# Kernel optimization log

Measured on AMD Instinct MI355X. Metric: run time of the kernel, lower is better.

Reference implementation:

```python
import jax, jax.numpy as jnp
import numpy as np

N_NODES = 100000
N_EDGES = 3200000
IN_CH = 32
EDGE_DIM = 8
HEADS = 8
HIDDEN = 64


def _lin(key, fan_in, fan_out, bias=True):
    k1, k2 = jax.random.split(key)
    s = 1.0 / np.sqrt(fan_in)
    w = jax.random.uniform(k1, (fan_in, fan_out), jnp.float32, -s, s)
    if bias:
        b = jax.random.uniform(k2, (fan_out,), jnp.float32, -s, s)
        return w, b
    return w


def setup_inputs() -> dict:
    key = jax.random.key(0)
    ks = jax.random.split(key, 40)
    inp = {}
    inp['x'] = jax.random.normal(ks[0], (N_NODES, IN_CH), jnp.float32)
    inp['edge_index'] = jax.random.randint(ks[1], (2, N_EDGES), 0, N_NODES, jnp.int32)
    inp['edge_attr'] = jax.random.normal(ks[2], (N_EDGES, EDGE_DIM), jnp.float32)
    # layer dims: (in, heads, out_per_head)
    dims = [(IN_CH, HEADS, 6), (HEADS * 6, HEADS, 3), (HEADS * 3, 1, HIDDEN)]
    ki = 3
    for li, (cin, H, C) in enumerate(dims, start=1):
        HC = H * C
        inp[f'wq{li}'], inp[f'bq{li}'] = _lin(ks[ki], cin, HC); ki += 1
        inp[f'wk{li}'], inp[f'bk{li}'] = _lin(ks[ki], cin, HC); ki += 1
        inp[f'wv{li}'], inp[f'bv{li}'] = _lin(ks[ki], cin, HC); ki += 1
        inp[f'we{li}'] = _lin(ks[ki], EDGE_DIM, HC, bias=False); ki += 1
        inp[f'wskip{li}'], inp[f'bskip{li}'] = _lin(ks[ki], cin, HC); ki += 1
        inp[f'wbeta{li}'] = _lin(ks[ki], 3 * HC, 1, bias=False); ki += 1
    inp['wc'], inp['bc'] = _lin(ks[ki], HIDDEN, 1)
    return inp


def _transformer_conv(x, src, dst, edge_attr, wq, bq, wk, bk, wv, bv, we, wskip, bskip, wbeta, H, C):
    """PyG TransformerConv (concat=True, beta=True, root_weight=True), eval mode."""
    N = x.shape[0]
    e = (edge_attr @ we).reshape(-1, H, C)                  # [E,H,C]
    q = (x @ wq + bq).reshape(N, H, C)[dst]                 # [E,H,C]
    k = (x @ wk + bk).reshape(N, H, C)[src] + e
    v = (x @ wv + bv).reshape(N, H, C)[src] + e
    logits = (q * k).sum(-1) * (1.0 / np.sqrt(C))           # [E,H]
    # segment softmax over incoming edges of each dst node
    m = jax.ops.segment_max(logits, dst, num_segments=N)
    ex = jnp.exp(logits - m[dst])
    den = jax.ops.segment_sum(ex, dst, num_segments=N)
    alpha = ex / (den[dst] + 1e-16)                         # [E,H]
    out = jax.ops.segment_sum(alpha[:, :, None] * v, dst, num_segments=N)
    out = out.reshape(N, H * C)
    x_r = x @ wskip + bskip
    g = jax.nn.sigmoid(jnp.concatenate([out, x_r, out - x_r], axis=-1) @ wbeta)  # [N,1]
    return g * x_r + (1.0 - g) * out


def reference(x, edge_index, edge_attr,
              wq1, bq1, wk1, bk1, wv1, bv1, we1, wskip1, bskip1, wbeta1,
              wq2, bq2, wk2, bk2, wv2, bv2, we2, wskip2, bskip2, wbeta2,
              wq3, bq3, wk3, bk3, wv3, bv3, we3, wskip3, bskip3, wbeta3,
              wc, bc):
    src, dst = edge_index[0], edge_index[1]
    h = _transformer_conv(x, src, dst, edge_attr, wq1, bq1, wk1, bk1, wv1, bv1, we1, wskip1, bskip1, wbeta1, HEADS, 6)
    h = jax.nn.relu(h)
    h = _transformer_conv(h, src, dst, edge_attr, wq2, bq2, wk2, bk2, wv2, bv2, we2, wskip2, bskip2, wbeta2, HEADS, 3)
    h = jax.nn.relu(h)
    h = _transformer_conv(h, src, dst, edge_attr, wq3, bq3, wk3, bk3, wv3, bv3, we3, wskip3, bskip3, wbeta3, 1, HIDDEN)
    h = jax.nn.relu(h)
    logits = (h @ wc + bc).squeeze(-1)                      # [N]
    return logits
```

## Files before the change

### kernel.cpp

```cpp
#include <hip/hip_runtime.h>
#include <hip/hip_fp16.h>
#include <math.h>

#define RCHUNK 8192
#define NBUCK 512
#define CAP 12288

__device__ __forceinline__ float2 H2F(unsigned u) {
    __half2 h = *reinterpret_cast<__half2*>(&u);
    return __half22float2(h);
}
__device__ __forceinline__ unsigned F2H(float a, float b) {
    __half2 h = __floats2half2_rn(a, b);
    return *reinterpret_cast<unsigned*>(&h);
}

__device__ __forceinline__ void loadA(const __half* p, float* a) {
    uint4 u = *(const uint4*)p;
    float2 t;
    t = H2F(u.x); a[0] = t.x; a[1] = t.y;
    t = H2F(u.y); a[2] = t.x; a[3] = t.y;
    t = H2F(u.z); a[4] = t.x; a[5] = t.y;
    t = H2F(u.w); a[6] = t.x; a[7] = t.y;
}

template<int C>
__device__ __forceinline__ void loadKV(const __half* p, float* k, float* v) {
    if constexpr (C == 6) {
        uint4 p0 = *(const uint4*)p;
        uint4 p1 = *(const uint4*)(p + 8);
        float2 t;
        t = H2F(p0.x); k[0] = t.x; k[1] = t.y;
        t = H2F(p0.y); k[2] = t.x; k[3] = t.y;
        t = H2F(p0.z); k[4] = t.x; k[5] = t.y;
        t = H2F(p0.w); v[0] = t.x; v[1] = t.y;
        t = H2F(p1.x); v[2] = t.x; v[3] = t.y;
        t = H2F(p1.y); v[4] = t.x; v[5] = t.y;
    } else {
        uint4 p0 = *(const uint4*)p;
        float2 t;
        t = H2F(p0.x); k[0] = t.x; k[1] = t.y;
        t = H2F(p0.y); k[2] = t.x; v[0] = t.y;
        t = H2F(p0.z); v[1] = t.x; v[2] = t.y;
    }
}

__global__ void histA_kernel(const int* __restrict__ ei, int* __restrict__ hist,
                             int E, int nblk) {
    __shared__ int h[NBUCK];
    h[threadIdx.x] = 0;
    h[threadIdx.x + 256] = 0;
    __syncthreads();
    int base = blockIdx.x * RCHUNK;
#pragma unroll
    for (int r = 0; r < RCHUNK / 256; ++r) {
        int i = base + r * 256 + threadIdx.x;
        if (i < E) atomicAdd(&h[ei[E + i] >> 8], 1);
    }
    __syncthreads();
    hist[threadIdx.x * nblk + blockIdx.x] = h[threadIdx.x];
    hist[(threadIdx.x + 256) * nblk + blockIdx.x] = h[threadIdx.x + 256];
}

__global__ void scanB_kernel(int* __restrict__ hist, int* __restrict__ btot, int nblk) {
    __shared__ int sm[1024];
    int b = blockIdx.x;
    int tid = threadIdx.x;
    int v = (tid < nblk) ? hist[b * nblk + tid] : 0;
    sm[tid] = v;
    __syncthreads();
    for (int off = 1; off < 1024; off <<= 1) {
        int t = (tid >= off) ? sm[tid - off] : 0;
        __syncthreads();
        sm[tid] += t;
        __syncthreads();
    }
    if (tid < nblk) hist[b * nblk + tid] = sm[tid] - v;
    if (tid == 1023) btot[b] = sm[1023];
}

__global__ void scanC_kernel(const int* __restrict__ btot, int* __restrict__ bbase) {
    __shared__ int sm[NBUCK];
    int tid = threadIdx.x;
    int v = btot[tid];
    sm[tid] = v;
    __syncthreads();
    for (int off = 1; off < NBUCK; off <<= 1) {
        int t = (tid >= off) ? sm[tid - off] : 0;
        __syncthreads();
        sm[tid] += t;
        __syncthreads();
    }
    bbase[tid] = sm[tid] - v;
}

__global__ void reorderB_kernel(const int* __restrict__ ei, const int* __restrict__ hist,
                                const int* __restrict__ bbase, unsigned* __restrict__ sorted,
                                int E, int nblk) {
    __shared__ int off[NBUCK];
    off[threadIdx.x] = bbase[threadIdx.x] + hist[threadIdx.x * nblk + blockIdx.x];
    off[threadIdx.x + 256] = bbase[threadIdx.x + 256] + hist[(threadIdx.x + 256) * nblk + blockIdx.x];
    __syncthreads();
    int base = blockIdx.x * RCHUNK;
#pragma unroll
    for (int r = 0; r < RCHUNK / 256; ++r) {
        int i = base + r * 256 + threadIdx.x;
        if (i < E) {
            int dst = ei[E + i];
            int k = atomicAdd(&off[dst >> 8], 1);
            sorted[k] = ((unsigned)(dst & 255) << 24) | (unsigned)i;
        }
    }
}

__global__ __launch_bounds__(256) void bucketsort_kernel(
        const unsigned* __restrict__ sorted,
        const int* __restrict__ bbase, const int* __restrict__ btot,
        int* __restrict__ rowptr,
        const int* __restrict__ ei, const float* __restrict__ ea,
        int* __restrict__ srcp, __half* __restrict__ eap, int N, int E) {
    __shared__ int h[256];
    __shared__ int tmp[CAP];
    int b = blockIdx.x;
    int lo = b << 8;
    int s = bbase[b], cnt = btot[b];
    int tid = threadIdx.x;

    h[tid] = 0;
    __syncthreads();
    for (int i = tid; i < cnt; i += 256) atomicAdd(&h[sorted[s + i] >> 24], 1);
    __syncthreads();
    int v = h[tid];
    for (int off = 1; off < 256; off <<= 1) {
        int t = (tid >= off) ? h[tid - off] : 0;
        __syncthreads();
        h[tid] += t;
        __syncthreads();
    }
    int excl = h[tid] - v;
    int dst = lo + tid;
    if (dst < N) rowptr[dst] = s + excl;
    if (b == 0 && tid == 0) rowptr[N] = E;
    __syncthreads();
    h[tid] = excl;
    __syncthreads();
    for (int i = tid; i < cnt; i += 256) {
        unsigned p2 = sorted[s + i];
        int dl = p2 >> 24;
        int eid = p2 & 0xFFFFFF;
        int r = atomicAdd(&h[dl], 1);
        if (r < CAP) {
            tmp[r] = eid;
        } else {
            int slot = s + r;
            srcp[slot] = ei[eid];
            float4 a0 = *(const float4*)(ea + (size_t)eid * 8);
            float4 a1 = *(const float4*)(ea + (size_t)eid * 8 + 4);
            uint4 u;
            u.x = F2H(a0.x, a0.y); u.y = F2H(a0.z, a0.w);
            u.z = F2H(a1.x, a1.y); u.w = F2H(a1.z, a1.w);
            *(uint4*)(eap + (size_t)slot * 8) = u;
        }
    }
    __syncthreads();
    int m = cnt < CAP ? cnt : CAP;
    for (int j = tid; j < m; j += 256) {
        int eid = tmp[j];
        int slot = s + j;
        srcp[slot] = ei[eid];
        float4 a0 = *(const float4*)(ea + (size_t)eid * 8);
        float4 a1 = *(const float4*)(ea + (size_t)eid * 8 + 4);
        uint4 u;
        u.x = F2H(a0.x, a0.y); u.y = F2H(a0.z, a0.w);
        u.z = F2H(a1.x, a1.y); u.w = F2H(a1.z, a1.w);
        *(uint4*)(eap + (size_t)slot * 8) = u;
    }
}

template<int CIN, int C, int PK>
__global__ void proj8_kernel(const float* __restrict__ X,
                             const float* __restrict__ wq, const float* __restrict__ bq,
                             const float* __restrict__ wk, const float* __restrict__ bk,
                             const float* __restrict__ wv, const float* __restrict__ bv,
                             const float* __restrict__ wsk, const float* __restrict__ bsk,
                             float* __restrict__ Q, __half* __restrict__ KV,
                             float* __restrict__ S, int N)
{
    const int HC = 8 * C;
    int idx = blockIdx.x * blockDim.x + threadIdx.x;
    if (idx >= N * HC) return;
    int n = idx / HC;
    int c = idx - n * HC;
    int h = c / C;
    int cc = c - h * C;
    float q = bq[c], k = bk[c], v = bv[c], s = bsk[c];
    const float* xr = X + (size_t)n * CIN;
#pragma unroll
    for (int i = 0; i < CIN; ++i) {
        float xi = xr[i];
        q = fmaf(xi, wq[i * HC + c], q);
        k = fmaf(xi, wk[i * HC + c], k);
        v = fmaf(xi, wv[i * HC + c], v);
        s = fmaf(xi, wsk[i * HC + c], s);
    }
    Q[(size_t)n * HC + c] = q;
    __half* kp = KV + (size_t)n * (8 * PK) + h * PK;
    kp[cc] = __float2half_rn(k);
    kp[C + cc] = __float2half_rn(v);
    S[(size_t)n * HC + c] = s;
}

__global__ void proj64_kernel(const float* __restrict__ X,
                              const float* __restrict__ wq, const float* __restrict__ bq,
                              const float* __restrict__ wk, const float* __restrict__ bk,
                              const float* __restrict__ wv, const float* __restrict__ bv,
                              const float* __restrict__ wsk, const float* __restrict__ bsk,
                              float* __restrict__ Q, __half* __restrict__ K16,
                              __half* __restrict__ V16, float* __restrict__ S, int N)
{
    int idx = blockIdx.x * blockDim.x + threadIdx.x;
    if (idx >= N * 64) return;
    int n = idx >> 6;
    int c = idx & 63;
    float q = bq[c], k = bk[c], v = bv[c], s = bsk[c];
    const float* xr = X + (size_t)n * 24;
#pragma unroll
    for (int i = 0; i < 24; ++i) {
        float xi = xr[i];
        q = fmaf(xi, wq[i * 64 + c], q);
        k = fmaf(xi, wk[i * 64 + c], k);
        v = fmaf(xi, wv[i * 64 + c], v);
        s = fmaf(xi, wsk[i * 64 + c], s);
    }
    Q[idx] = q;
    K16[idx] = __float2half_rn(k);
    V16[idx] = __float2half_rn(v);
    S[idx] = s;
}

template<int C, int PK, int UNR>
__global__ void gather8f_kernel(const int* __restrict__ rowptr,
                                const int* __restrict__ srcp,
                                const __half* __restrict__ eap,
                                const float* __restrict__ we,
                                const float* __restrict__ Q,
                                const __half* __restrict__ KV,
                                const float* __restrict__ S,
                                const float* __restrict__ wb,
                                float* __restrict__ OUT,
                                int N, float scale)
{
    const int HC = 8 * C;
    int tid = blockIdx.x * blockDim.x + threadIdx.x;
    int n = tid >> 3;
    int h = tid & 7;
    if (n >= N) return;

    float q[C];
    const float* Qp = Q + (size_t)n * HC + h * C;
#pragma unroll
    for (int c = 0; c < C; ++c) q[c] = Qp[c];

    float qe[8];
#pragma unroll
    for (int d = 0; d < 8; ++d) {
        float t = 0.f;
#pragma unroll
        for (int c = 0; c < C; ++c) t = fmaf(we[d * HC + h * C + c], q[c], t);
        qe[d] = t;
    }

    float num[C];
#pragma unroll
    for (int c = 0; c < C; ++c) num[c] = 0.f;
    float sacc[8];
#pragma unroll
    for (int d = 0; d < 8; ++d) sacc[d] = 0.f;
    float den = 0.f;

    int rs = rowptr[n], re = rowptr[n + 1];
    int j = rs;
    for (; j + UNR - 1 < re; j += UNR) {
        int se[UNR];
        float a[UNR][8], kk[UNR][C], vv[UNR][C];
#pragma unroll
        for (int u = 0; u < UNR; ++u) se[u] = srcp[j + u];
#pragma unroll
        for (int u = 0; u < UNR; ++u) loadA(eap + (size_t)(j + u) * 8, a[u]);
#pragma unroll
        for (int u = 0; u < UNR; ++u)
            loadKV<C>(KV + (size_t)se[u] * (8 * PK) + h * PK, kk[u], vv[u]);
        float ex[UNR];
#pragma unroll
        for (int u = 0; u < UNR; ++u) {
            float d0 = 0.f;
#pragma unroll
            for (int c = 0; c < C; ++c) d0 = fmaf(q[c], kk[u][c], d0);
            float qa = 0.f;
#pragma unroll
            for (int d = 0; d < 8; ++d) qa = fmaf(qe[d], a[u][d], qa);
            ex[u] = __expf((d0 + qa) * scale);
        }
#pragma unroll
        for (int u = 0; u < UNR; ++u) {
            den += ex[u];
#pragma unroll
            for (int c = 0; c < C; ++c) num[c] = fmaf(ex[u], vv[u][c], num[c]);
#pragma unroll
            for (int d = 0; d < 8; ++d) sacc[d] = fmaf(ex[u], a[u][d], sacc[d]);
        }
    }
    for (; j < re; ++j) {
        int s0 = srcp[j];
        float a0[8];
        loadA(eap + (size_t)j * 8, a0);
        float k0[C], v0[C];
        loadKV<C>(KV + (size_t)s0 * (8 * PK) + h * PK, k0, v0);
        float d0 = 0.f;
#pragma unroll
        for (int c = 0; c < C; ++c) d0 = fmaf(q[c], k0[c], d0);
        float qa0 = 0.f;
#pragma unroll
        for (int d = 0; d < 8; ++d) qa0 = fmaf(qe[d], a0[d], qa0);
        float ex0 = __expf((d0 + qa0) * scale);
        den += ex0;
#pragma unroll
        for (int c = 0; c < C; ++c) num[c] = fmaf(ex0, v0[c], num[c]);
#pragma unroll
        for (int d = 0; d < 8; ++d) sacc[d] = fmaf(ex0, a0[d], sacc[d]);
    }

    float inv = 1.f / (den + 1e-16f);
    float outc[C], sc[C];
    float gd = 0.f;
#pragma unroll
    for (int c = 0; c < C; ++c) {
        float e_ = 0.f;
#pragma unroll
        for (int d = 0; d < 8; ++d) e_ = fmaf(we[d * HC + h * C + c], sacc[d], e_);
        float o = (num[c] + e_) * inv;
        float s_ = S[(size_t)n * HC + h * C + c];
        outc[c] = o;
        sc[c] = s_;
        gd += o * wb[h * C + c] + s_ * wb[HC + h * C + c] + (o - s_) * wb[2 * HC + h * C + c];
    }
    gd += __shfl_xor(gd, 1, 8);
    gd += __shfl_xor(gd, 2, 8);
    gd += __shfl_xor(gd, 4, 8);
    float g = 1.f / (1.f + __expf(-gd));
#pragma unroll
    for (int c = 0; c < C; ++c) {
        float hh = fmaxf(g * sc[c] + (1.f - g) * outc[c], 0.f);
        OUT[(size_t)n * HC + h * C + c] = hh;
    }
}

__global__ __launch_bounds__(256) void gather64f_kernel(
        const int* __restrict__ rowptr,
        const int* __restrict__ srcp,
        const __half* __restrict__ eap,
        const float* __restrict__ we,
        const float* __restrict__ Q,
        const __half* __restrict__ K16,
        const __half* __restrict__ V16,
        const float* __restrict__ S,
        const float* __restrict__ wb,
        const float* __restrict__ wc,
        const float* __restrict__ bc,
        float* __restrict__ OUT,
        int N, float scale)
{
    int grp = (blockIdx.x * blockDim.x + threadIdx.x) >> 3;
    int l8 = threadIdx.x & 7;
    if (grp >= N) return;
    int c0 = l8 << 3;

    float q[8];
    *(float4*)q       = *(const float4*)(Q + (size_t)grp * 64 + c0);
    *(float4*)(q + 4) = *(const float4*)(Q + (size_t)grp * 64 + c0 + 4);
    float qe[8];
#pragma unroll
    for (int d = 0; d < 8; ++d) {
        float4 w0 = *(const float4*)(we + d * 64 + c0);
        float4 w1 = *(const float4*)(we + d * 64 + c0 + 4);
        float t = w0.x * q[0];
        t = fmaf(w0.y, q[1], t); t = fmaf(w0.z, q[2], t); t = fmaf(w0.w, q[3], t);
        t = fmaf(w1.x, q[4], t); t = fmaf(w1.y, q[5], t); t = fmaf(w1.z, q[6], t);
        t = fmaf(w1.w, q[7], t);
        qe[d] = t;
    }

    float num[8];
#pragma unroll
    for (int c = 0; c < 8; ++c) num[c] = 0.f;
    float sacc[8];
#pragma unroll
    for (int d = 0; d < 8; ++d) sacc[d] = 0.f;
    float den = 0.f;

    int rs = rowptr[grp], re = rowptr[grp + 1];
    int j = rs;
    for (; j + 3 < re; j += 4) {
        int se[4];
        float a[4][8];
        uint4 ku[4], vu[4];
#pragma unroll
        for (int u = 0; u < 4; ++u) se[u] = srcp[j + u];
#pragma unroll
        for (int u = 0; u < 4; ++u) loadA(eap + (size_t)(j + u) * 8, a[u]);
#pragma unroll
        for (int u = 0; u < 4; ++u) {
            ku[u] = *(const uint4*)(K16 + (size_t)se[u] * 64 + c0);
            vu[u] = *(const uint4*)(V16 + (size_t)se[u] * 64 + c0);
        }
        float t[4];
#pragma unroll
        for (int u = 0; u < 4; ++u) {
            float2 k01 = H2F(ku[u].x), k23 = H2F(ku[u].y);
            float2 k45 = H2F(ku[u].z), k67 = H2F(ku[u].w);
            float tt = q[0] * k01.x;
            tt = fmaf(q[1], k01.y, tt); tt = fmaf(q[2], k23.x, tt);
            tt = fmaf(q[3], k23.y, tt); tt = fmaf(q[4], k45.x, tt);
            tt = fmaf(q[5], k45.y, tt); tt = fmaf(q[6], k67.x, tt);
            tt = fmaf(q[7], k67.y, tt);
#pragma unroll
            for (int d = 0; d < 8; ++d) tt = fmaf(qe[d], a[u][d], tt);
            t[u] = tt;
        }
#pragma unroll
        for (int off = 4; off > 0; off >>= 1) {
            t[0] += __shfl_xor(t[0], off, 8);
            t[1] += __shfl_xor(t[1], off, 8);
            t[2] += __shfl_xor(t[2], off, 8);
            t[3] += __shfl_xor(t[3], off, 8);
        }
#pragma unroll
        for (int u = 0; u < 4; ++u) {
            float ex = __expf(t[u] * scale);
            den += ex;
            float2 v01 = H2F(vu[u].x), v23 = H2F(vu[u].y);
            float2 v45 = H2F(vu[u].z), v67 = H2F(vu[u].w);
            num[0] = fmaf(ex, v01.x, num[0]);
            num[1] = fmaf(ex, v01.y, num[1]);
            num[2] = fmaf(ex, v23.x, num[2]);
            num[3] = fmaf(ex, v23.y, num[3]);
            num[4] = fmaf(ex, v45.x, num[4]);
            num[5] = fmaf(ex, v45.y, num[5]);
            num[6] = fmaf(ex, v67.x, num[6]);
            num[7] = fmaf(ex, v67.y, num[7]);
#pragma unroll
            for (int d = 0; d < 8; ++d) sacc[d] = fmaf(ex, a[u][d], sacc[d]);
        }
    }
    for (; j < re; ++j) {
        int s0 = srcp[j];
        float a0[8];
        loadA(eap + (size_t)j * 8, a0);
        uint4 ku0 = *(const uint4*)(K16 + (size_t)s0 * 64 + c0);
        uint4 vu0 = *(const uint4*)(V16 + (size_t)s0 * 64 + c0);
        float2 k01 = H2F(ku0.x), k23 = H2F(ku0.y);
        float2 k45 = H2F(ku0.z), k67 = H2F(ku0.w);
        float t0 = q[0] * k01.x;
        t0 = fmaf(q[1], k01.y, t0); t0 = fmaf(q[2], k23.x, t0);
        t0 = fmaf(q[3], k23.y, t0); t0 = fmaf(q[4], k45.x, t0);
        t0 = fmaf(q[5], k45.y, t0); t0 = fmaf(q[6], k67.x, t0);
        t0 = fmaf(q[7], k67.y, t0);
#pragma unroll
        for (int d = 0; d < 8; ++d) t0 = fmaf(qe[d], a0[d], t0);
#pragma unroll
        for (int off = 4; off > 0; off >>= 1) t0 += __shfl_xor(t0, off, 8);
        float ex0 = __expf(t0 * scale);
        den += ex0;
        float2 v01 = H2F(vu0.x), v23 = H2F(vu0.y);
        float2 v45 = H2F(vu0.z), v67 = H2F(vu0.w);
        num[0] = fmaf(ex0, v01.x, num[0]);
        num[1] = fmaf(ex0, v01.y, num[1]);
        num[2] = fmaf(ex0, v23.x, num[2]);
        num[3] = fmaf(ex0, v23.y, num[3]);
        num[4] = fmaf(ex0, v45.x, num[4]);
        num[5] = fmaf(ex0, v45.y, num[5]);
        num[6] = fmaf(ex0, v67.x, num[6]);
        num[7] = fmaf(ex0, v67.y, num[7]);
#pragma unroll
        for (int d = 0; d < 8; ++d) sacc[d] = fmaf(ex0, a0[d], sacc[d]);
    }

#pragma unroll
    for (int d = 0; d < 8; ++d) {
        float4 w0 = *(const float4*)(we + d * 64 + c0);
        float4 w1 = *(const float4*)(we + d * 64 + c0 + 4);
        num[0] = fmaf(w0.x, sacc[d], num[0]);
        num[1] = fmaf(w0.y, sacc[d], num[1]);
        num[2] = fmaf(w0.z, sacc[d], num[2]);
        num[3] = fmaf(w0.w, sacc[d], num[3]);
        num[4] = fmaf(w1.x, sacc[d], num[4]);
        num[5] = fmaf(w1.y, sacc[d], num[5]);
        num[6] = fmaf(w1.z, sacc[d], num[6]);
        num[7] = fmaf(w1.w, sacc[d], num[7]);
    }
    float inv = 1.f / (den + 1e-16f);
    float o[8], sv[8];
    *(float4*)sv       = *(const float4*)(S + (size_t)grp * 64 + c0);
    *(float4*)(sv + 4) = *(const float4*)(S + (size_t)grp * 64 + c0 + 4);
    float gd = 0.f;
#pragma unroll
    for (int c = 0; c < 8; ++c) {
        o[c] = num[c] * inv;
        gd += o[c] * wb[c0 + c] + sv[c] * wb[64 + c0 + c] + (o[c] - sv[c]) * wb[128 + c0 + c];
    }
#pragma unroll
    for (int off = 4; off > 0; off >>= 1) gd += __shfl_xor(gd, off, 8);
    float g = 1.f / (1.f + __expf(-gd));
    float t = 0.f;
#pragma unroll
    for (int c = 0; c < 8; ++c) {
        float hh = fmaxf(g * sv[c] + (1.f - g) * o[c], 0.f);
        t = fmaf(hh, wc[c0 + c], t);
    }
#pragma unroll
    for (int off = 4; off > 0; off >>= 1) t += __shfl_xor(t, off, 8);
    if (l8 == 0) OUT[grp] = t + bc[0];
}

extern "C" void kernel_launch(void* const* d_in, const int* in_sizes, int n_in,
                              void* d_out, int out_size, void* d_ws, size_t ws_size,
                              hipStream_t stream) {
    const float* x  = (const float*)d_in[0];
    const int*   ei = (const int*)d_in[1];
    const float* ea = (const float*)d_in[2];
    const int N = in_sizes[0] / 32;
    const int E = in_sizes[1] / 2;

    int p = 3;
    const float *wq1=(const float*)d_in[p+0], *bq1=(const float*)d_in[p+1],
                *wk1=(const float*)d_in[p+2], *bk1=(const float*)d_in[p+3],
                *wv1=(const float*)d_in[p+4], *bv1=(const float*)d_in[p+5],
                *we1=(const float*)d_in[p+6],
                *wsk1=(const float*)d_in[p+7], *bsk1=(const float*)d_in[p+8],
                *wb1=(const float*)d_in[p+9];
    p += 10;
    const float *wq2=(const float*)d_in[p+0], *bq2=(const float*)d_in[p+1],
                *wk2=(const float*)d_in[p+2], *bk2=(const float*)d_in[p+3],
                *wv2=(const float*)d_in[p+4], *bv2=(const float*)d_in[p+5],
                *we2=(const float*)d_in[p+6],
                *wsk2=(const float*)d_in[p+7], *bsk2=(const float*)d_in[p+8],
                *wb2=(const float*)d_in[p+9];
    p += 10;
    const float *wq3=(const float*)d_in[p+0], *bq3=(const float*)d_in[p+1],
                *wk3=(const float*)d_in[p+2], *bk3=(const float*)d_in[p+3],
                *wv3=(const float*)d_in[p+4], *bv3=(const float*)d_in[p+5],
                *we3=(const float*)d_in[p+6],
                *wsk3=(const float*)d_in[p+7], *bsk3=(const float*)d_in[p+8],
                *wb3=(const float*)d_in[p+9];
    p += 10;
    const float *wc = (const float*)d_in[p+0], *bc = (const float*)d_in[p+1];

    float* out = (float*)d_out;

    float* ws = (float*)d_ws;
    float* Hb = ws;
    float* Qb = Hb + (size_t)N * 48;
    float* Sb = Qb + (size_t)N * 64;
    __half* KV16  = (__half*)(Sb + (size_t)N * 64);
    __half* K3    = KV16;
    __half* V3    = KV16 + (size_t)N * 64;
    __half* eap16 = KV16 + (size_t)N * 128;
    int* ip      = (int*)(eap16 + (size_t)E * 8);
    int* rowptr  = ip;
    int* btot    = rowptr + (N + 2);
    int* bbase   = btot + 512;
    int* srcp    = bbase + 512;
    int* hist    = srcp + E;
    unsigned* sorted = (unsigned*)Qb;

    const int BLK = 256;
    const int nblkR = (E + RCHUNK - 1) / RCHUNK;
    const int nbuckUsed = (N + 255) >> 8;

    histA_kernel<<<nblkR, 256, 0, stream>>>(ei, hist, E, nblkR);
    scanB_kernel<<<NBUCK, 1024, 0, stream>>>(hist, btot, nblkR);
    scanC_kernel<<<1, NBUCK, 0, stream>>>(btot, bbase);
    reorderB_kernel<<<nblkR, 256, 0, stream>>>(ei, hist, bbase, sorted, E, nblkR);
    bucketsort_kernel<<<nbuckUsed, 256, 0, stream>>>(
        sorted, bbase, btot, rowptr, ei, ea, srcp, eap16, N, E);

    proj8_kernel<32,6,16><<<(N*48 + BLK-1)/BLK, BLK, 0, stream>>>(
        x, wq1,bq1, wk1,bk1, wv1,bv1, wsk1,bsk1, Qb, KV16, Sb, N);
    gather8f_kernel<6,16,2><<<(N*8 + BLK-1)/BLK, BLK, 0, stream>>>(
        rowptr, srcp, eap16, we1, Qb, KV16, Sb, wb1, Hb, N, 1.0f/sqrtf(6.0f));

    proj8_kernel<48,3,8><<<(N*24 + BLK-1)/BLK, BLK, 0, stream>>>(
        Hb, wq2,bq2, wk2,bk2, wv2,bv2, wsk2,bsk2, Qb, KV16, Sb, N);
    gather8f_kernel<3,8,4><<<(N*8 + BLK-1)/BLK, BLK, 0, stream>>>(
        rowptr, srcp, eap16, we2, Qb, KV16, Sb, wb2, Hb, N, 1.0f/sqrtf(3.0f));

    proj64_kernel<<<(N*64 + BLK-1)/BLK, BLK, 0, stream>>>(
        Hb, wq3,bq3, wk3,bk3, wv3,bv3, wsk3,bsk3, Qb, K3, V3, Sb, N);
    gather64f_kernel<<<((size_t)N*8 + BLK-1)/BLK, BLK, 0, stream>>>(
        rowptr, srcp, eap16, we3, Qb, K3, V3, Sb, wb3, wc, bc, out, N, 1.0f/8.0f);
}
```

Before: 794.6 us.

## Fuse layer-1 projection into reorder kernel and interleave layer-3 K/V rows

Merges the edge reorder pass and the layer-1 Q/K/V/skip projection into one launch using disjoint block ranges. This removes a kernel launch and lets the two independent workloads overlap on the GPU. The sorted buffer moves out of Qb into its own workspace region so it no longer aliases the projection output. Layer-3 K and V are now stored interleaved per node, so each gathered source row's K and V are fetched from one contiguous 256-byte line instead of two separate arrays. This needs extra workspace space and assumes the workspace is large enough.

```diff
diff --git a/kernel.cpp b/kernel.cpp
--- a/kernel.cpp
+++ b/kernel.cpp
@@ -94,23 +94,56 @@
     bbase[tid] = sm[tid] - v;
 }
 
-__global__ void reorderB_kernel(const int* __restrict__ ei, const int* __restrict__ hist,
-                                const int* __restrict__ bbase, unsigned* __restrict__ sorted,
-                                int E, int nblk) {
-    __shared__ int off[NBUCK];
-    off[threadIdx.x] = bbase[threadIdx.x] + hist[threadIdx.x * nblk + blockIdx.x];
-    off[threadIdx.x + 256] = bbase[threadIdx.x + 256] + hist[(threadIdx.x + 256) * nblk + blockIdx.x];
-    __syncthreads();
-    int base = blockIdx.x * RCHUNK;
-#pragma unroll
-    for (int r = 0; r < RCHUNK / 256; ++r) {
-        int i = base + r * 256 + threadIdx.x;
-        if (i < E) {
-            int dst = ei[E + i];
-            int k = atomicAdd(&off[dst >> 8], 1);
-            sorted[k] = ((unsigned)(dst & 255) << 24) | (unsigned)i;
-        }
-    }
+__global__ void reorder_proj_kernel(const int* __restrict__ ei, const int* __restrict__ hist,
+                                    const int* __restrict__ bbase, unsigned* __restrict__ sorted,
+                                    int E, int nblk,
+                                    const float* __restrict__ X,
+                                    const float* __restrict__ wq, const float* __restrict__ bq,
+                                    const float* __restrict__ wk, const float* __restrict__ bk,
+                                    const float* __restrict__ wv, const float* __restrict__ bv,
+                                    const float* __restrict__ wsk, const float* __restrict__ bsk,
+                                    float* __restrict__ Q, __half* __restrict__ KV,
+                                    float* __restrict__ S, int N)
+{
+    if (blockIdx.x < (unsigned)nblk) {
+        __shared__ int off[NBUCK];
+        off[threadIdx.x] = bbase[threadIdx.x] + hist[threadIdx.x * nblk + blockIdx.x];
+        off[threadIdx.x + 256] = bbase[threadIdx.x + 256] + hist[(threadIdx.x + 256) * nblk + blockIdx.x];
+        __syncthreads();
+        int base = blockIdx.x * RCHUNK;
+#pragma unroll
+        for (int r = 0; r < RCHUNK / 256; ++r) {
+            int i = base + r * 256 + threadIdx.x;
+            if (i < E) {
+                int dst = ei[E + i];
+                int k = atomicAdd(&off[dst >> 8], 1);
+                sorted[k] = ((unsigned)(dst & 255) << 24) | (unsigned)i;
+            }
+        }
+        return;
+    }
+    const int HC = 48;
+    int idx = (blockIdx.x - nblk) * blockDim.x + threadIdx.x;
+    if (idx >= N * HC) return;
+    int n = idx / HC;
+    int c = idx - n * HC;
+    int h = c / 6;
+    int cc = c - h * 6;
+    float q = bq[c], k = bk[c], v = bv[c], s = bsk[c];
+    const float* xr = X + (size_t)n * 32;
+#pragma unroll
+    for (int i = 0; i < 32; ++i) {
+        float xi = xr[i];
+        q = fmaf(xi, wq[i * HC + c], q);
+        k = fmaf(xi, wk[i * HC + c], k);
+        v = fmaf(xi, wv[i * HC + c], v);
+        s = fmaf(xi, wsk[i * HC + c], s);
+    }
+    Q[(size_t)n * HC + c] = q;
+    __half* kp = KV + (size_t)n * 128 + h * 16;
+    kp[cc] = __float2half_rn(k);
+    kp[6 + cc] = __float2half_rn(v);
+    S[(size_t)n * HC + c] = s;
 }
 
 __global__ __launch_bounds__(256) void bucketsort_kernel(
@@ -215,8 +248,8 @@
                               const float* __restrict__ wk, const float* __restrict__ bk,
                               const float* __restrict__ wv, const float* __restrict__ bv,
                               const float* __restrict__ wsk, const float* __restrict__ bsk,
-                              float* __restrict__ Q, __half* __restrict__ K16,
-                              __half* __restrict__ V16, float* __restrict__ S, int N)
+                              float* __restrict__ Q, __half* __restrict__ KV3,
+                              float* __restrict__ S, int N)
 {
     int idx = blockIdx.x * blockDim.x + threadIdx.x;
     if (idx >= N * 64) return;
@@ -233,8 +266,9 @@
         s = fmaf(xi, wsk[i * 64 + c], s);
     }
     Q[idx] = q;
-    K16[idx] = __float2half_rn(k);
-    V16[idx] = __float2half_rn(v);
+    __half* kp = KV3 + (size_t)n * 128;
+    kp[c] = __float2half_rn(k);
+    kp[64 + c] = __float2half_rn(v);
     S[idx] = s;
 }
 
@@ -361,8 +395,7 @@
         const __half* __restrict__ eap,
         const float* __restrict__ we,
         const float* __restrict__ Q,
-        const __half* __restrict__ K16,
-        const __half* __restrict__ V16,
+        const __half* __restrict__ KV3,
         const float* __restrict__ S,
         const float* __restrict__ wb,
         const float* __restrict__ wc,
@@ -410,8 +443,9 @@
         for (int u = 0; u < 4; ++u) loadA(eap + (size_t)(j + u) * 8, a[u]);
 #pragma unroll
         for (int u = 0; u < 4; ++u) {
-            ku[u] = *(const uint4*)(K16 + (size_t)se[u] * 64 + c0);
-            vu[u] = *(const uint4*)(V16 + (size_t)se[u] * 64 + c0);
+            const __half* kvp = KV3 + (size_t)se[u] * 128;
+            ku[u] = *(const uint4*)(kvp + c0);
+            vu[u] = *(const uint4*)(kvp + 64 + c0);
         }
         float t[4];
 #pragma unroll
@@ -456,8 +490,9 @@
         int s0 = srcp[j];
         float a0[8];
         loadA(eap + (size_t)j * 8, a0);
-        uint4 ku0 = *(const uint4*)(K16 + (size_t)s0 * 64 + c0);
-        uint4 vu0 = *(const uint4*)(V16 + (size_t)s0 * 64 + c0);
+        const __half* kvp = KV3 + (size_t)s0 * 128;
+        uint4 ku0 = *(const uint4*)(kvp + c0);
+        uint4 vu0 = *(const uint4*)(kvp + 64 + c0);
         float2 k01 = H2F(ku0.x), k23 = H2F(ku0.y);
         float2 k45 = H2F(ku0.z), k67 = H2F(ku0.w);
         float t0 = q[0] * k01.x;
@@ -562,8 +597,7 @@
     float* Qb = Hb + (size_t)N * 48;
     float* Sb = Qb + (size_t)N * 64;
     __half* KV16  = (__half*)(Sb + (size_t)N * 64);
-    __half* K3    = KV16;
-    __half* V3    = KV16 + (size_t)N * 64;
+    __half* KV3   = KV16;
     __half* eap16 = KV16 + (size_t)N * 128;
     int* ip      = (int*)(eap16 + (size_t)E * 8);
     int* rowptr  = ip;
@@ -571,21 +605,24 @@
     int* bbase   = btot + 512;
     int* srcp    = bbase + 512;
     int* hist    = srcp + E;
-    unsigned* sorted = (unsigned*)Qb;
+    const int nblkR = (E + RCHUNK - 1) / RCHUNK;
+    unsigned* sorted = (unsigned*)(hist + (size_t)NBUCK * nblkR);
 
     const int BLK = 256;
-    const int nblkR = (E + RCHUNK - 1) / RCHUNK;
     const int nbuckUsed = (N + 255) >> 8;
 
     histA_kernel<<<nblkR, 256, 0, stream>>>(ei, hist, E, nblkR);
     scanB_kernel<<<NBUCK, 1024, 0, stream>>>(hist, btot, nblkR);
     scanC_kernel<<<1, NBUCK, 0, stream>>>(btot, bbase);
-    reorderB_kernel<<<nblkR, 256, 0, stream>>>(ei, hist, bbase, sorted, E, nblkR);
+    {
+        int projBlocks = (N * 48 + BLK - 1) / BLK;
+        reorder_proj_kernel<<<nblkR + projBlocks, 256, 0, stream>>>(
+            ei, hist, bbase, sorted, E, nblkR,
+            x, wq1, bq1, wk1, bk1, wv1, bv1, wsk1, bsk1, Qb, KV16, Sb, N);
+    }
     bucketsort_kernel<<<nbuckUsed, 256, 0, stream>>>(
         sorted, bbase, btot, rowptr, ei, ea, srcp, eap16, N, E);
 
-    proj8_kernel<32,6,16><<<(N*48 + BLK-1)/BLK, BLK, 0, stream>>>(
-        x, wq1,bq1, wk1,bk1, wv1,bv1, wsk1,bsk1, Qb, KV16, Sb, N);
     gather8f_kernel<6,16,2><<<(N*8 + BLK-1)/BLK, BLK, 0, stream>>>(
         rowptr, srcp, eap16, we1, Qb, KV16, Sb, wb1, Hb, N, 1.0f/sqrtf(6.0f));
 
@@ -595,7 +632,7 @@
         rowptr, srcp, eap16, we2, Qb, KV16, Sb, wb2, Hb, N, 1.0f/sqrtf(3.0f));
 
     proj64_kernel<<<(N*64 + BLK-1)/BLK, BLK, 0, stream>>>(
-        Hb, wq3,bq3, wk3,bk3, wv3,bv3, wsk3,bsk3, Qb, K3, V3, Sb, N);
+        Hb, wq3,bq3, wk3,bk3, wv3,bv3, wsk3,bsk3, Qb, KV3, Sb, N);
     gather64f_kernel<<<((size_t)N*8 + BLK-1)/BLK, BLK, 0, stream>>>(
-        rowptr, srcp, eap16, we3, Qb, K3, V3, Sb, wb3, wc, bc, out, N, 1.0f/8.0f);
-}
+        rowptr, srcp, eap16, we3, Qb, KV3, Sb, wb3, wc, bc, out, N, 1.0f/8.0f);
+}
```

New measurement: 786.1 us (median of 2 runs). About the same (-1.1%).
